# Kernel tuning notes

Measured on AMD Instinct MI355X. Metric: run time of the kernel, lower is better.

The kernel has to match this reference:

```python
import jax, jax.numpy as jnp
import numpy as np

EMBEDDINGS = 16
DENSE = 256
HEAD_SIZE = 64


def setup_inputs() -> dict:
    key = jax.random.key(0)
    ks = jax.random.split(key, 7)
    B, T = 4096, 100
    x = jax.random.normal(ks[0], (B, T, EMBEDDINGS), dtype=jnp.float32)
    s1 = EMBEDDINGS ** -0.5
    s2 = HEAD_SIZE ** -0.5
    # Linear weights stored as [in, out] (torch stores transposed; math identical)
    Wk = jax.random.uniform(ks[1], (EMBEDDINGS, HEAD_SIZE), jnp.float32, -s1, s1)
    Wq = jax.random.uniform(ks[2], (EMBEDDINGS, HEAD_SIZE), jnp.float32, -s1, s1)
    Wv = jax.random.uniform(ks[3], (EMBEDDINGS, HEAD_SIZE), jnp.float32, -s1, s1)
    Wdk = jax.random.uniform(ks[4], (HEAD_SIZE, DENSE), jnp.float32, -s2, s2)
    Wdq = jax.random.uniform(ks[5], (HEAD_SIZE, DENSE), jnp.float32, -s2, s2)
    Wdv = jax.random.uniform(ks[6], (HEAD_SIZE, DENSE), jnp.float32, -s2, s2)
    return {"x": x, "Wk": Wk, "Wq": Wq, "Wv": Wv, "Wdk": Wdk, "Wdq": Wdq, "Wdv": Wdv}


def reference(x, Wk, Wq, Wv, Wdk, Wdq, Wdv):
    B, T, C = x.shape
    # two chained bias-free projections per stream: [B,T,C] -> [B,T,H] -> [B,T,DENSE]
    k = (x @ Wk) @ Wdk
    q = (x @ Wq) @ Wdq
    v = (x @ Wv) @ Wdv
    # NOTE: original scales by C**-0.5 where C is the INPUT embedding dim (16)
    wei = jnp.einsum("btd,bsd->bts", q, k) * (C ** -0.5)  # [B,T,T]
    causal = jnp.tril(jnp.ones((T, T), dtype=bool))
    wei = jnp.where(causal, wei, -jnp.inf)
    wei = jax.nn.softmax(wei, axis=-1)
    # dropout omitted (eval-mode reference; training dropout is stochastic)
    out = wei @ v  # [B,T,DENSE]
    return out
```

## Files before the change

### kernel.cpp

```cpp
#include <hip/hip_runtime.h>

#define T_SEQ 100
#define C_EMB 16
#define DCOL  256


__global__ __launch_bounds__(256) void prep_kernel(
    const float* __restrict__ Wk, const float* __restrict__ Wq,
    const float* __restrict__ Wv, const float* __restrict__ Wdk,
    const float* __restrict__ Wdq, const float* __restrict__ Wdv,
    float* __restrict__ ws)
{
    __shared__ float WQL[16][260];
    __shared__ float WKL[16][260];
    const int tid = threadIdx.x;

    for (int i = 0; i < 16; ++i) {
        float aq = 0.f, ak = 0.f;
        for (int h = 0; h < 64; ++h) {
            aq += Wq[i*64 + h] * Wdq[h*256 + tid];
            ak += Wk[i*64 + h] * Wdk[h*256 + tid];
        }
        WQL[i][tid >> 4 == 0 ? tid : tid] = aq;
        WQL[i][tid] = aq;
        WKL[i][tid] = ak;
    }
    __syncthreads();

    {
        const float scale = 0.25f * 1.4426950408889634f;
        const int k = tid >> 4;
        const int c = tid & 15;
        float acc = 0.f;
        for (int d = 0; d < 256; ++d)
            acc += WQL[k][d] * WKL[c][d];
        ws[k*16 + c] = acc * scale;
    }

    for (int c = 0; c < 16; ++c) {
        float acc = 0.f;
        for (int h = 0; h < 64; ++h)
            acc += Wv[c*64 + h] * Wdv[h*256 + tid];
        ws[256 + c*256 + tid] = acc;
    }
}

__global__ __launch_bounds__(128) void attn_kernel(
    const float* __restrict__ x, const float* __restrict__ ws,
    float* __restrict__ out)
{
    __shared__ float Zs[T_SEQ * 16];

    const int b   = blockIdx.x;
    const int tid = threadIdx.x;
    const int t   = tid;
    const int wid = tid >> 6;

    const float* __restrict__ xb = x + (size_t)b * (T_SEQ * C_EMB);

    const int tl = (t < T_SEQ) ? t : (T_SEQ - 1);
    float xt[16];
    {
        const float4* xr = (const float4*)(xb + tl * 16);
        #pragma unroll
        for (int i = 0; i < 4; ++i) {
            float4 q = xr[i];
            xt[4*i+0] = q.x; xt[4*i+1] = q.y; xt[4*i+2] = q.z; xt[4*i+3] = q.w;
        }
    }

    float y[16];
    #pragma unroll
    for (int c = 0; c < 16; ++c) y[c] = 0.f;
    #pragma unroll
    for (int k = 0; k < 16; ++k) {
        const float xk = xt[k];
        #pragma unroll
        for (int c = 0; c < 16; ++c)
            y[c] += xk * ws[k*16 + c];
    }

    float z[16];
    #pragma unroll
    for (int c = 0; c < 16; ++c) z[c] = 0.f;
    float l = 0.f;

    const int smax = (wid == 0) ? 64 : T_SEQ;
    for (int s = 0; s < smax; ++s) {
        float sx[16];
        {
            const float4* xr = (const float4*)(xb + s * 16);
            #pragma unroll
            for (int i = 0; i < 4; ++i) {
                float4 q = xr[i];
                sx[4*i+0] = q.x; sx[4*i+1] = q.y; sx[4*i+2] = q.z; sx[4*i+3] = q.w;
            }
        }
        float sc = 0.f;
        #pragma unroll
        for (int c = 0; c < 16; ++c) sc += y[c] * sx[c];
        float p = __builtin_amdgcn_exp2f(sc);
        p = (s <= t) ? p : 0.f;
        l += p;
        #pragma unroll
        for (int c = 0; c < 16; ++c) z[c] += p * sx[c];
    }

    if (t < T_SEQ) {
        const float li = __builtin_amdgcn_rcpf(l);
        #pragma unroll
        for (int i = 0; i < 4; ++i) {
            float4 q;
            q.x = z[4*i+0] * li; q.y = z[4*i+1] * li;
            q.z = z[4*i+2] * li; q.w = z[4*i+3] * li;
            ((float4*)&Zs[t * 16])[i] = q;
        }
    }
    __syncthreads();

    const int j = tid & 63;
    const float* __restrict__ WVp = ws + 256;
    float wv[16][4];
    #pragma unroll
    for (int c = 0; c < 16; ++c)
        #pragma unroll
        for (int g = 0; g < 4; ++g)
            wv[c][g] = WVp[c*256 + g*64 + j];

    float* __restrict__ outb = out + (size_t)b * (T_SEQ * DCOL);
    for (int tt = wid; tt < T_SEQ; tt += 2) {
        float zr[16];
        #pragma unroll
        for (int i = 0; i < 4; ++i) {
            float4 q = ((const float4*)&Zs[tt * 16])[i];
            zr[4*i+0] = q.x; zr[4*i+1] = q.y; zr[4*i+2] = q.z; zr[4*i+3] = q.w;
        }
        float acc[4] = {0.f, 0.f, 0.f, 0.f};
        #pragma unroll
        for (int c = 0; c < 16; ++c)
            #pragma unroll
            for (int g = 0; g < 4; ++g)
                acc[g] += zr[c] * wv[c][g];
        #pragma unroll
        for (int g = 0; g < 4; ++g)
            outb[tt*256 + g*64 + j] = acc[g];
    }
}

extern "C" void kernel_launch(void* const* d_in, const int* in_sizes, int n_in,
                              void* d_out, int out_size, void* d_ws, size_t ws_size,
                              hipStream_t stream) {
    const float* x   = (const float*)d_in[0];
    const float* Wk  = (const float*)d_in[1];
    const float* Wq  = (const float*)d_in[2];
    const float* Wv  = (const float*)d_in[3];
    const float* Wdk = (const float*)d_in[4];
    const float* Wdq = (const float*)d_in[5];
    const float* Wdv = (const float*)d_in[6];
    float* out = (float*)d_out;
    float* ws  = (float*)d_ws;

    const int B = in_sizes[0] / (T_SEQ * C_EMB);

    prep_kernel<<<1, 256, 0, stream>>>(Wk, Wq, Wv, Wdk, Wdq, Wdv, ws);
    attn_kernel<<<B, 128, 0, stream>>>(x, ws, out);
}
```

Before: 641.7 us.

## Stage x in LDS, vectorize output stores, restructure weight prep kernel

The attention kernel now copies each batch's x tile into shared memory once and reads it from LDS inside the key loop, where it previously re-read global memory on every iteration. The output projection loads WV as float4 and writes contiguous float4 stores per thread instead of strided scalar stores. The prep kernel fuses the three weight products into one pass over h with register accumulators and uses float4 LDS reads for the Q·K fold. The costs are an extra 6.4KB of shared memory per block and an additional barrier.

```diff
diff --git a/kernel.cpp b/kernel.cpp
--- a/kernel.cpp
+++ b/kernel.cpp
@@ -15,15 +15,25 @@
     __shared__ float WKL[16][260];
     const int tid = threadIdx.x;
 
+    float aq[16], ak[16], av[16];
+    #pragma unroll
+    for (int i = 0; i < 16; ++i) { aq[i] = 0.f; ak[i] = 0.f; av[i] = 0.f; }
+    for (int h = 0; h < 64; ++h) {
+        const float wdq = Wdq[h*256 + tid];
+        const float wdk = Wdk[h*256 + tid];
+        const float wdv = Wdv[h*256 + tid];
+        #pragma unroll
+        for (int i = 0; i < 16; ++i) {
+            aq[i] += Wq[i*64 + h] * wdq;
+            ak[i] += Wk[i*64 + h] * wdk;
+            av[i] += Wv[i*64 + h] * wdv;
+        }
+    }
+    #pragma unroll
     for (int i = 0; i < 16; ++i) {
-        float aq = 0.f, ak = 0.f;
-        for (int h = 0; h < 64; ++h) {
-            aq += Wq[i*64 + h] * Wdq[h*256 + tid];
-            ak += Wk[i*64 + h] * Wdk[h*256 + tid];
-        }
-        WQL[i][tid >> 4 == 0 ? tid : tid] = aq;
-        WQL[i][tid] = aq;
-        WKL[i][tid] = ak;
+        WQL[i][tid] = aq[i];
+        WKL[i][tid] = ak[i];
+        ws[256 + i*256 + tid] = av[i];
     }
     __syncthreads();
 
@@ -32,16 +42,12 @@
         const int k = tid >> 4;
         const int c = tid & 15;
         float acc = 0.f;
-        for (int d = 0; d < 256; ++d)
-            acc += WQL[k][d] * WKL[c][d];
+        for (int d4 = 0; d4 < 64; ++d4) {
+            float4 a = *(const float4*)&WQL[k][4*d4];
+            float4 b = *(const float4*)&WKL[c][4*d4];
+            acc += a.x*b.x + a.y*b.y + a.z*b.z + a.w*b.w;
+        }
         ws[k*16 + c] = acc * scale;
-    }
-
-    for (int c = 0; c < 16; ++c) {
-        float acc = 0.f;
-        for (int h = 0; h < 64; ++h)
-            acc += Wv[c*64 + h] * Wdv[h*256 + tid];
-        ws[256 + c*256 + tid] = acc;
     }
 }
 
@@ -49,6 +55,7 @@
     const float* __restrict__ x, const float* __restrict__ ws,
     float* __restrict__ out)
 {
+    __shared__ float Xs[T_SEQ * 16];
     __shared__ float Zs[T_SEQ * 16];
 
     const int b   = blockIdx.x;
@@ -58,15 +65,16 @@
 
     const float* __restrict__ xb = x + (size_t)b * (T_SEQ * C_EMB);
 
+    for (int i = tid; i < T_SEQ * 4; i += 128)
+        ((float4*)Xs)[i] = ((const float4*)xb)[i];
+    __syncthreads();
+
     const int tl = (t < T_SEQ) ? t : (T_SEQ - 1);
     float xt[16];
-    {
-        const float4* xr = (const float4*)(xb + tl * 16);
-        #pragma unroll
-        for (int i = 0; i < 4; ++i) {
-            float4 q = xr[i];
-            xt[4*i+0] = q.x; xt[4*i+1] = q.y; xt[4*i+2] = q.z; xt[4*i+3] = q.w;
-        }
+    #pragma unroll
+    for (int i = 0; i < 4; ++i) {
+        float4 q = ((const float4*)&Xs[tl * 16])[i];
+        xt[4*i+0] = q.x; xt[4*i+1] = q.y; xt[4*i+2] = q.z; xt[4*i+3] = q.w;
     }
 
     float y[16];
@@ -88,13 +96,10 @@
     const int smax = (wid == 0) ? 64 : T_SEQ;
     for (int s = 0; s < smax; ++s) {
         float sx[16];
-        {
-            const float4* xr = (const float4*)(xb + s * 16);
-            #pragma unroll
-            for (int i = 0; i < 4; ++i) {
-                float4 q = xr[i];
-                sx[4*i+0] = q.x; sx[4*i+1] = q.y; sx[4*i+2] = q.z; sx[4*i+3] = q.w;
-            }
+        #pragma unroll
+        for (int i = 0; i < 4; ++i) {
+            float4 q = ((const float4*)&Xs[s * 16])[i];
+            sx[4*i+0] = q.x; sx[4*i+1] = q.y; sx[4*i+2] = q.z; sx[4*i+3] = q.w;
         }
         float sc = 0.f;
         #pragma unroll
@@ -120,12 +125,10 @@
 
     const int j = tid & 63;
     const float* __restrict__ WVp = ws + 256;
-    float wv[16][4];
+    float4 wv[16];
     #pragma unroll
     for (int c = 0; c < 16; ++c)
-        #pragma unroll
-        for (int g = 0; g < 4; ++g)
-            wv[c][g] = WVp[c*256 + g*64 + j];
+        wv[c] = *(const float4*)&WVp[c*256 + 4*j];
 
     float* __restrict__ outb = out + (size_t)b * (T_SEQ * DCOL);
     for (int tt = wid; tt < T_SEQ; tt += 2) {
@@ -135,15 +138,15 @@
             float4 q = ((const float4*)&Zs[tt * 16])[i];
             zr[4*i+0] = q.x; zr[4*i+1] = q.y; zr[4*i+2] = q.z; zr[4*i+3] = q.w;
         }
-        float acc[4] = {0.f, 0.f, 0.f, 0.f};
+        float4 acc = make_float4(0.f, 0.f, 0.f, 0.f);
         #pragma unroll
-        for (int c = 0; c < 16; ++c)
-            #pragma unroll
-            for (int g = 0; g < 4; ++g)
-                acc[g] += zr[c] * wv[c][g];
-        #pragma unroll
-        for (int g = 0; g < 4; ++g)
-            outb[tt*256 + g*64 + j] = acc[g];
+        for (int c = 0; c < 16; ++c) {
+            acc.x += zr[c] * wv[c].x;
+            acc.y += zr[c] * wv[c].y;
+            acc.z += zr[c] * wv[c].z;
+            acc.w += zr[c] * wv[c].w;
+        }
+        *(float4*)&outb[tt*256 + 4*j] = acc;
     }
 }
 
```

Measured after the change: 563.1 us. 1.14x faster.
